# Performance work log

Hardware: AMD Instinct MI355X
Metric: run time of the kernel (lower is better)

## Reference

```python
import jax, jax.numpy as jnp
import numpy as np

NUM_EMBEDDINGS = 4096
EMBEDDING_DIM = 64
COMMITMENT_COST = 0.25
DECAY = 0.99
EPS = 1e-5


def setup_inputs() -> dict:
    key = jax.random.key(0)
    k1, k2, k3 = jax.random.split(key, 3)
    z = jax.random.normal(k1, (32, 1024, EMBEDDING_DIM), dtype=jnp.float32)
    # codebook initialized uniform(-1/K, 1/K) in the original; use small-scale normal-equivalent uniform
    embedding = jax.random.uniform(k2, (NUM_EMBEDDINGS, EMBEDDING_DIM), dtype=jnp.float32,
                                   minval=-1.0 / NUM_EMBEDDINGS, maxval=1.0 / NUM_EMBEDDINGS)
    ema_cluster_size = jnp.zeros((NUM_EMBEDDINGS,), dtype=jnp.float32)
    ema_w = embedding  # buffer initialized as a clone of the weight
    return {"z": z, "embedding": embedding, "ema_cluster_size": ema_cluster_size, "ema_w": ema_w}


def reference(z, embedding, ema_cluster_size, ema_w):
    B, T, D = z.shape
    K = embedding.shape[0]
    z_flat = z.reshape(-1, D)  # [N, D], N = B*T

    # squared L2 distances: ||z||^2 + ||e||^2 - 2 z e^T  -> [N, K]
    d = (jnp.sum(z_flat * z_flat, axis=1, keepdims=True)
         + jnp.sum(embedding * embedding, axis=1)
         - 2.0 * jnp.einsum('nd,kd->nk', z_flat, embedding))
    indices = jnp.argmin(d, axis=1)  # [N]

    z_q = embedding[indices].reshape(B, T, D)

    # EMA codebook update (training path); segment_sum == one-hot matmul, without
    # materializing the [N, K] one-hot matrix.
    counts = jax.ops.segment_sum(jnp.ones_like(indices, dtype=jnp.float32), indices,
                                 num_segments=K)  # encodings.sum(0)
    dw = jax.ops.segment_sum(z_flat, indices, num_segments=K)  # (z_flat^T @ encodings)^T -> [K, D]
    new_cluster_size = DECAY * ema_cluster_size + (1.0 - DECAY) * counts
    new_ema_w = DECAY * ema_w + (1.0 - DECAY) * dw
    n = jnp.sum(new_cluster_size)
    cluster_size = (new_cluster_size + EPS) / (n + K * EPS) * n
    new_embedding = new_ema_w / cluster_size[:, None]

    commitment_loss = COMMITMENT_COST * jnp.mean((z - jax.lax.stop_gradient(z_q)) ** 2)
    z_q_st = z + jax.lax.stop_gradient(z_q - z)  # straight-through estimator
    return (z_q_st, indices.reshape(B, T), commitment_loss,
            new_embedding, new_cluster_size, new_ema_w)
```

## Files before the change

kernel.cpp:

```cpp
#include <hip/hip_runtime.h>

#define N_ROWS 32768
#define K_EMB  4096
#define D_DIM  64
#define MARGIN 5e-4f
#define CAND_CAP 16
#define NQ      4
#define KC_CH   256
#define CH_PER  (K_EMB / NQ / KC_CH)

#define WS_EE     0
#define WS_BEST   4096
#define WS_IDX    69632
#define WS_COUNTS 102400
#define WS_DW     106496
#define WS_LOSS   368640
#define WS_N      368641
#define F_BHI     368644
#define F_BLO     499716
#define F_ROWMIN  630788
#define F_CNT     663556
#define F_CAND    696324
#define WS_NEED_BYTES ((size_t)(696324 + 32768 * CAND_CAP) * 4)

#define O_ZQ    0
#define O_IDX   2097152
#define O_LOSS  2129920
#define O_EMB   2129921
#define O_CS    2392065
#define O_EMAW  2396161

typedef __attribute__((ext_vector_type(8))) short short8;
typedef __attribute__((ext_vector_type(4))) float f32x4;

__device__ __forceinline__ unsigned short f2bf(float f) {
    unsigned u = __float_as_uint(f);
    unsigned r = (u + 0x7FFFu + ((u >> 16) & 1u)) >> 16;
    return (unsigned short)r;
}
__device__ __forceinline__ unsigned keyf(float f) {
    unsigned u = __float_as_uint(f);
    return (u & 0x80000000u) ? ~u : (u | 0x80000000u);
}
__device__ __forceinline__ float keyinv(unsigned k) {
    unsigned u = (k & 0x80000000u) ? (k ^ 0x80000000u) : ~k;
    return __uint_as_float(u);
}

__global__ void k_ee(const float* __restrict__ emb, float* __restrict__ ee) {
    int k = blockIdx.x * 256 + threadIdx.x;
    const float4* e4 = (const float4*)(emb + (size_t)k * D_DIM);
    float s0 = 0.f, s1 = 0.f, s2 = 0.f, s3 = 0.f;
#pragma unroll
    for (int i = 0; i < 16; ++i) {
        float4 v = e4[i];
        s0 = fmaf(v.x, v.x, s0);
        s1 = fmaf(v.y, v.y, s1);
        s2 = fmaf(v.z, v.z, s2);
        s3 = fmaf(v.w, v.w, s3);
    }
    ee[k] = (s0 + s1) + (s2 + s3);
}

__global__ void k_prep(const float* __restrict__ emb, float* __restrict__ ee,
                       unsigned short* __restrict__ bhi)
{
    int k = blockIdx.x * 256 + threadIdx.x;
    const float4* e4 = (const float4*)(emb + (size_t)k * D_DIM);
    float s0 = 0.f, s1 = 0.f, s2 = 0.f, s3 = 0.f;
    unsigned short* bh = bhi + (size_t)k * D_DIM;
#pragma unroll
    for (int i = 0; i < 16; ++i) {
        float4 v = e4[i];
        s0 = fmaf(v.x, v.x, s0);
        s1 = fmaf(v.y, v.y, s1);
        s2 = fmaf(v.z, v.z, s2);
        s3 = fmaf(v.w, v.w, s3);
        bh[4 * i + 0] = f2bf(v.x);
        bh[4 * i + 1] = f2bf(v.y);
        bh[4 * i + 2] = f2bf(v.z);
        bh[4 * i + 3] = f2bf(v.w);
    }
    ee[k] = (s0 + s1) + (s2 + s3);
}

template <int PASS>
__global__ __launch_bounds__(256, 2) void k_mfma_pass(
    const float* __restrict__ z, const unsigned short* __restrict__ bhi,
    const float* __restrict__ ee,
    unsigned* __restrict__ rowmin, unsigned* __restrict__ cnt, int* __restrict__ cand)
{
    __shared__ unsigned short lds_b[KC_CH * 64];
    __shared__ float lds_e2[KC_CH];

    const int tid  = threadIdx.x;
    const int lane = tid & 63, wave = tid >> 6;
    const int lrow = lane & 15, lgrp = lane >> 4;
    const int row0   = blockIdx.x * 256 + wave * 64;
    const int kquart = blockIdx.y * (K_EMB / NQ);

    short8 Ah[4][2];
#pragma unroll
    for (int s = 0; s < 4; ++s) {
#pragma unroll
        for (int t = 0; t < 2; ++t) {
            const float* zp = z + (size_t)(row0 + s * 16 + lrow) * D_DIM + t * 32 + lgrp * 8;
            float4 f0 = *(const float4*)zp;
            float4 f1 = *(const float4*)(zp + 4);
            float zf[8] = {f0.x, f0.y, f0.z, f0.w, f1.x, f1.y, f1.z, f1.w};
            short8 h;
#pragma unroll
            for (int j = 0; j < 8; ++j) h[j] = (short)f2bf(zf[j]);
            Ah[s][t] = h;
        }
    }

    float track[4][4];
#pragma unroll
    for (int s = 0; s < 4; ++s)
#pragma unroll
        for (int r = 0; r < 4; ++r) {
            track[s][r] = (PASS == 1)
                ? -3.4e38f
                : -0.5f * (keyinv(rowmin[row0 + s * 16 + lgrp * 4 + r]) + MARGIN);
        }

    const int swz = lrow & 7;

    for (int ch = 0; ch < CH_PER; ++ch) {
        const int kbase = kquart + ch * KC_CH;

        __syncthreads();
        {
            const short8* gsrc = (const short8*)(bhi + (size_t)kbase * D_DIM);
            short8 v[8];
#pragma unroll
            for (int j = 0; j < 8; ++j) v[j] = gsrc[tid + j * 256];
            const int s_slot = tid & 7, c0 = tid >> 3;
#pragma unroll
            for (int j = 0; j < 8; ++j) {
                int c = c0 + j * 32;
                *(short8*)&lds_b[c * 64 + ((s_slot ^ (c & 7)) << 3)] = v[j];
            }
            lds_e2[tid & (KC_CH - 1)] = -0.5f * ee[kbase + (tid & (KC_CH - 1))];
        }
        __syncthreads();

#pragma unroll 2
        for (int kt = 0; kt < KC_CH / 32; ++kt) {
            short8 B0[2], B1[2];
            float  e2[2];
#pragma unroll
            for (int u = 0; u < 2; ++u) {
                const int c = kt * 32 + u * 16 + lrow;
                B0[u] = *(const short8*)&lds_b[c * 64 + ((lgrp ^ swz) << 3)];
                B1[u] = *(const short8*)&lds_b[c * 64 + (((lgrp + 4) ^ swz) << 3)];
                e2[u] = lds_e2[c];
            }
#pragma unroll
            for (int s = 0; s < 4; ++s) {
#pragma unroll
                for (int u = 0; u < 2; ++u) {
                    f32x4 acc = {e2[u], e2[u], e2[u], e2[u]};
                    acc = __builtin_amdgcn_mfma_f32_16x16x32_bf16(Ah[s][0], B0[u], acc, 0, 0, 0);
                    acc = __builtin_amdgcn_mfma_f32_16x16x32_bf16(Ah[s][1], B1[u], acc, 0, 0, 0);
#pragma unroll
                    for (int r = 0; r < 4; ++r) {
                        if (PASS == 1) {
                            track[s][r] = fmaxf(track[s][r], acc[r]);
                        } else {
                            if (acc[r] > track[s][r]) {
                                int row = row0 + s * 16 + lgrp * 4 + r;
                                unsigned slot = atomicAdd(&cnt[row], 1u);
                                if (slot < (unsigned)CAND_CAP)
                                    cand[(size_t)row * CAND_CAP + slot] =
                                        kbase + kt * 32 + u * 16 + lrow;
                            }
                        }
                    }
                }
            }
        }
    }

    if (PASS == 1) {
#pragma unroll
        for (int s = 0; s < 4; ++s)
#pragma unroll
            for (int r = 0; r < 4; ++r) {
                float v = track[s][r];
                v = fmaxf(v, __shfl_xor(v, 1));
                v = fmaxf(v, __shfl_xor(v, 2));
                v = fmaxf(v, __shfl_xor(v, 4));
                v = fmaxf(v, __shfl_xor(v, 8));
                if (lrow == 0)
                    atomicMin(&rowmin[row0 + s * 16 + lgrp * 4 + r], keyf(-2.0f * v));
            }
    }
}

__global__ void k_refine(const float* __restrict__ z, const float* __restrict__ emb,
                         const float* __restrict__ ee, const unsigned* __restrict__ cnt,
                         const int* __restrict__ cand, unsigned long long* __restrict__ best)
{
    int row = blockIdx.x * 256 + threadIdx.x;
    const float4* zp = (const float4*)(z + (size_t)row * D_DIM);

    float s0 = 0.f, s1 = 0.f, s2 = 0.f, s3 = 0.f;
#pragma unroll
    for (int i = 0; i < 16; ++i) {
        float4 v = zp[i];
        s0 = fmaf(v.x, v.x, s0);
        s1 = fmaf(v.y, v.y, s1);
        s2 = fmaf(v.z, v.z, s2);
        s3 = fmaf(v.w, v.w, s3);
    }
    const float zz = (s0 + s1) + (s2 + s3);

    int c = (int)cnt[row];
    if (c > CAND_CAP) c = CAND_CAP;
    unsigned long long bk = 0xFFFFFFFFFFFFFFFFull;
    for (int i = 0; i < c; ++i) {
        int k = cand[(size_t)row * CAND_CAP + i];
        const float4* ep = (const float4*)(emb + (size_t)k * D_DIM);
        float d0 = 0.f, d1 = 0.f, d2 = 0.f, d3 = 0.f;
#pragma unroll
        for (int j = 0; j < 16; ++j) {
            float4 zv = zp[j];
            float4 ev = ep[j];
            d0 = fmaf(zv.x, ev.x, d0);
            d1 = fmaf(zv.y, ev.y, d1);
            d2 = fmaf(zv.z, ev.z, d2);
            d3 = fmaf(zv.w, ev.w, d3);
        }
        float dot = (d0 + d1) + (d2 + d3);
        float dv  = fmaf(-2.0f, dot, zz + ee[k]);
        unsigned long long key =
            ((unsigned long long)__float_as_uint(dv) << 32) | (unsigned)k;
        bk = (key < bk) ? key : bk;
    }
    best[row] = bk;
}

#define NCHUNK_FB 16
#define KC_FB     (K_EMB / NCHUNK_FB)
__global__ __launch_bounds__(256) void k_argmin_fb(
    const float* __restrict__ z, const float* __restrict__ emb,
    const float* __restrict__ ee, unsigned long long* __restrict__ best)
{
    const int n  = blockIdx.x * 256 + threadIdx.x;
    const int c  = blockIdx.y;
    const int k0 = c * KC_FB;

    float4 zr[16];
    const float4* zp = (const float4*)(z + (size_t)n * D_DIM);
#pragma unroll
    for (int i = 0; i < 16; ++i) zr[i] = zp[i];

    float s0 = 0.f, s1 = 0.f, s2 = 0.f, s3 = 0.f;
#pragma unroll
    for (int i = 0; i < 16; ++i) {
        s0 = fmaf(zr[i].x, zr[i].x, s0);
        s1 = fmaf(zr[i].y, zr[i].y, s1);
        s2 = fmaf(zr[i].z, zr[i].z, s2);
        s3 = fmaf(zr[i].w, zr[i].w, s3);
    }
    const float zz = (s0 + s1) + (s2 + s3);

    const float4* ep  = (const float4*)(emb + (size_t)k0 * D_DIM);
    const float*  eep = ee + k0;

    float bestv = 3.4e38f;
    int   bi    = 0;
#pragma unroll 2
    for (int kk = 0; kk < KC_FB; ++kk) {
        float d0 = 0.f, d1 = 0.f, d2 = 0.f, d3 = 0.f;
#pragma unroll
        for (int i = 0; i < 16; ++i) {
            float4 ev = ep[kk * 16 + i];
            d0 = fmaf(zr[i].x, ev.x, d0);
            d1 = fmaf(zr[i].y, ev.y, d1);
            d2 = fmaf(zr[i].z, ev.z, d2);
            d3 = fmaf(zr[i].w, ev.w, d3);
        }
        float dot = (d0 + d1) + (d2 + d3);
        float dv = fmaf(-2.0f, dot, zz + eep[kk]);
        if (dv < bestv) { bestv = dv; bi = kk; }
    }
    unsigned long long key =
        ((unsigned long long)__float_as_uint(bestv) << 32) | (unsigned)(k0 + bi);
    atomicMin(best + n, key);
}

__global__ void k_finish(const unsigned long long* __restrict__ best,
                         int* __restrict__ idxbuf, float* __restrict__ oidx)
{
    int n = blockIdx.x * 256 + threadIdx.x;
    int bi = (int)(best[n] & 0xFFFFFFFFull);
    idxbuf[n] = bi;
    oidx[n]   = (float)bi;
}

__global__ void k_scatter(const float* __restrict__ z, const float* __restrict__ emb,
                          const int* __restrict__ idxbuf, float* __restrict__ out_zq,
                          float* __restrict__ counts, float* __restrict__ dw,
                          float* __restrict__ lossacc)
{
    int t = blockIdx.x * 256 + threadIdx.x;
    float acc = 0.f;
#pragma unroll
    for (int i = 0; i < 16; ++i) {
        int e = t + i * 131072;
        int nrow = e >> 6, d = e & 63;
        int k = idxbuf[nrow];
        float zv  = z[e];
        float evv = emb[(size_t)k * D_DIM + d];
        out_zq[e] = zv + (evv - zv);
        float diff = zv - evv;
        acc = fmaf(diff, diff, acc);
        atomicAdd(&dw[(size_t)k * D_DIM + d], zv);
        if (d == 0) atomicAdd(&counts[k], 1.0f);
    }
    __shared__ float red[256];
    red[threadIdx.x] = acc;
    __syncthreads();
    for (int s = 128; s > 0; s >>= 1) {
        if (threadIdx.x < s) red[threadIdx.x] += red[threadIdx.x + s];
        __syncthreads();
    }
    if (threadIdx.x == 0) atomicAdd(lossacc, red[0]);
}

__global__ void k_stats(const float* __restrict__ ema_cs, const float* __restrict__ counts,
                        const float* __restrict__ lossacc, float* __restrict__ out_cs,
                        float* __restrict__ out_loss, float* __restrict__ ws_n)
{
    __shared__ float red[256];
    float local = 0.f;
    for (int k = threadIdx.x; k < K_EMB; k += 256) {
        float v = 0.99f * ema_cs[k] + 0.01f * counts[k];
        out_cs[k] = v;
        local += v;
    }
    red[threadIdx.x] = local;
    __syncthreads();
    for (int s = 128; s > 0; s >>= 1) {
        if (threadIdx.x < s) red[threadIdx.x] += red[threadIdx.x + s];
        __syncthreads();
    }
    if (threadIdx.x == 0) {
        ws_n[0] = red[0];
        out_loss[0] = 0.25f * (lossacc[0] / 2097152.0f);
    }
}

__global__ void k_emb(const float* __restrict__ ema_w, const float* __restrict__ dw,
                      const float* __restrict__ out_cs, const float* __restrict__ ws_n,
                      float* __restrict__ out_emb, float* __restrict__ out_emaw)
{
    int e = blockIdx.x * 256 + threadIdx.x;
    int k = e >> 6;
    float nv = ws_n[0];
    float w  = 0.99f * ema_w[e] + 0.01f * dw[e];
    out_emaw[e] = w;
    float cs = (out_cs[k] + 1e-5f) / (nv + 0.04096f) * nv;
    out_emb[e] = w / cs;
}

extern "C" void kernel_launch(void* const* d_in, const int* in_sizes, int n_in,
                              void* d_out, int out_size, void* d_ws, size_t ws_size,
                              hipStream_t stream)
{
    const float* z      = (const float*)d_in[0];
    const float* emb    = (const float*)d_in[1];
    const float* ema_cs = (const float*)d_in[2];
    const float* ema_w  = (const float*)d_in[3];

    float* out   = (float*)d_out;
    float* o_zq  = out + O_ZQ;
    float* o_idx = out + O_IDX;
    float* o_ls  = out + O_LOSS;
    float* o_em  = out + O_EMB;
    float* o_cs  = out + O_CS;
    float* o_ew  = out + O_EMAW;

    float* w      = (float*)d_ws;
    float* ee     = w + WS_EE;
    unsigned long long* best = (unsigned long long*)(w + WS_BEST);
    int*   idxbuf = (int*)(w + WS_IDX);
    float* counts = w + WS_COUNTS;
    float* dw     = w + WS_DW;
    float* lossa  = w + WS_LOSS;
    float* ws_n   = w + WS_N;

    hipMemsetAsync((char*)d_ws + (size_t)WS_BEST * 4, 0xFF, (size_t)N_ROWS * 8, stream);
    hipMemsetAsync((char*)d_ws + (size_t)WS_COUNTS * 4, 0,
                   (size_t)(WS_N + 1 - WS_COUNTS) * 4, stream);

    if (ws_size >= WS_NEED_BYTES) {
        unsigned short* bhi = (unsigned short*)(w + F_BHI);
        unsigned* rowmin    = (unsigned*)(w + F_ROWMIN);
        unsigned* cnt       = (unsigned*)(w + F_CNT);
        int*      cand      = (int*)(w + F_CAND);

        hipMemsetAsync((char*)d_ws + (size_t)F_ROWMIN * 4, 0xFF, (size_t)N_ROWS * 4, stream);
        hipMemsetAsync((char*)d_ws + (size_t)F_CNT * 4, 0, (size_t)N_ROWS * 4, stream);

        k_prep<<<K_EMB / 256, 256, 0, stream>>>(emb, ee, bhi);
        k_mfma_pass<1><<<dim3(N_ROWS / 256, NQ), 256, 0, stream>>>(z, bhi, ee,
                                                                   rowmin, cnt, cand);
        k_mfma_pass<2><<<dim3(N_ROWS / 256, NQ), 256, 0, stream>>>(z, bhi, ee,
                                                                   rowmin, cnt, cand);
        k_refine<<<N_ROWS / 256, 256, 0, stream>>>(z, emb, ee, cnt, cand, best);
    } else {
        k_ee<<<K_EMB / 256, 256, 0, stream>>>(emb, ee);
        k_argmin_fb<<<dim3(N_ROWS / 256, NCHUNK_FB), 256, 0, stream>>>(z, emb, ee, best);
    }

    k_finish<<<N_ROWS / 256, 256, 0, stream>>>(best, idxbuf, o_idx);
    k_scatter<<<512, 256, 0, stream>>>(z, emb, idxbuf, o_zq, counts, dw, lossa);
    k_stats<<<1, 256, 0, stream>>>(ema_cs, counts, lossa, o_cs, o_ls, ws_n);
    k_emb<<<(K_EMB * D_DIM) / 256, 256, 0, stream>>>(ema_w, dw, o_cs, ws_n, o_em, o_ew);
}
```

Baseline: 159.7 us.

## Fuse two MFMA distance passes into one kernel with per-quarter thresholds and rescue path

The separate max-pass and candidate-pass kernels are merged into one k_scan kernel. It computes each row's local best within its codebook quarter, then rescans the same quarter and keeps candidates within a margin of that local best. This drops the global rowmin buffer, its memset, the atomicMin and one launch, and shrinks blocks to 128 rows with launch_bounds 3 for occupancy. Because thresholds are now per-quarter, more candidates can be emitted per row. Rows that overflow the candidate cap go to a rescue list and get an exact full-codebook argmin in a new k_rescue kernel, which adds atomic traffic and an extra launch.

```diff
diff --git a/kernel.cpp b/kernel.cpp
--- a/kernel.cpp
+++ b/kernel.cpp
@@ -5,9 +5,11 @@
 #define D_DIM  64
 #define MARGIN 5e-4f
 #define CAND_CAP 16
+#define RESCUE_CAP 2048
 #define NQ      4
 #define KC_CH   256
 #define CH_PER  (K_EMB / NQ / KC_CH)
+#define ROWS_BLK 128
 
 #define WS_EE     0
 #define WS_BEST   4096
@@ -18,7 +20,7 @@
 #define WS_N      368641
 #define F_BHI     368644
 #define F_BLO     499716
-#define F_ROWMIN  630788
+#define F_RESCUE  630788
 #define F_CNT     663556
 #define F_CAND    696324
 #define WS_NEED_BYTES ((size_t)(696324 + 32768 * CAND_CAP) * 4)
@@ -37,14 +39,6 @@
     unsigned u = __float_as_uint(f);
     unsigned r = (u + 0x7FFFu + ((u >> 16) & 1u)) >> 16;
     return (unsigned short)r;
-}
-__device__ __forceinline__ unsigned keyf(float f) {
-    unsigned u = __float_as_uint(f);
-    return (u & 0x80000000u) ? ~u : (u | 0x80000000u);
-}
-__device__ __forceinline__ float keyinv(unsigned k) {
-    unsigned u = (k & 0x80000000u) ? (k ^ 0x80000000u) : ~k;
-    return __uint_as_float(u);
 }
 
 __global__ void k_ee(const float* __restrict__ emb, float* __restrict__ ee) {
@@ -84,11 +78,10 @@
     ee[k] = (s0 + s1) + (s2 + s3);
 }
 
-template <int PASS>
-__global__ __launch_bounds__(256, 2) void k_mfma_pass(
+__global__ __launch_bounds__(256, 3) void k_scan(
     const float* __restrict__ z, const unsigned short* __restrict__ bhi,
     const float* __restrict__ ee,
-    unsigned* __restrict__ rowmin, unsigned* __restrict__ cnt, int* __restrict__ cand)
+    unsigned* __restrict__ cnt, int* __restrict__ cand, unsigned* __restrict__ rescue)
 {
     __shared__ unsigned short lds_b[KC_CH * 64];
     __shared__ float lds_e2[KC_CH];
@@ -96,12 +89,12 @@
     const int tid  = threadIdx.x;
     const int lane = tid & 63, wave = tid >> 6;
     const int lrow = lane & 15, lgrp = lane >> 4;
-    const int row0   = blockIdx.x * 256 + wave * 64;
-    const int kquart = blockIdx.y * (K_EMB / NQ);
-
-    short8 Ah[4][2];
-#pragma unroll
-    for (int s = 0; s < 4; ++s) {
+    const int row0  = blockIdx.x * ROWS_BLK + wave * 32;
+    const int qbase = blockIdx.y * (K_EMB / NQ);
+
+    short8 Ah[2][2];
+#pragma unroll
+    for (int s = 0; s < 2; ++s) {
 #pragma unroll
         for (int t = 0; t < 2; ++t) {
             const float* zp = z + (size_t)(row0 + s * 16 + lrow) * D_DIM + t * 32 + lgrp * 8;
@@ -115,21 +108,15 @@
         }
     }
 
-    float track[4][4];
-#pragma unroll
-    for (int s = 0; s < 4; ++s)
-#pragma unroll
-        for (int r = 0; r < 4; ++r) {
-            track[s][r] = (PASS == 1)
-                ? -3.4e38f
-                : -0.5f * (keyinv(rowmin[row0 + s * 16 + lgrp * 4 + r]) + MARGIN);
-        }
-
     const int swz = lrow & 7;
+    float track[2][4];
+#pragma unroll
+    for (int s = 0; s < 2; ++s)
+#pragma unroll
+        for (int r = 0; r < 4; ++r) track[s][r] = -3.4e38f;
 
     for (int ch = 0; ch < CH_PER; ++ch) {
-        const int kbase = kquart + ch * KC_CH;
-
+        const int kbase = qbase + ch * KC_CH;
         __syncthreads();
         {
             const short8* gsrc = (const short8*)(bhi + (size_t)kbase * D_DIM);
@@ -158,44 +145,84 @@
                 e2[u] = lds_e2[c];
             }
 #pragma unroll
-            for (int s = 0; s < 4; ++s) {
+            for (int s = 0; s < 2; ++s)
 #pragma unroll
                 for (int u = 0; u < 2; ++u) {
                     f32x4 acc = {e2[u], e2[u], e2[u], e2[u]};
                     acc = __builtin_amdgcn_mfma_f32_16x16x32_bf16(Ah[s][0], B0[u], acc, 0, 0, 0);
                     acc = __builtin_amdgcn_mfma_f32_16x16x32_bf16(Ah[s][1], B1[u], acc, 0, 0, 0);
 #pragma unroll
+                    for (int r = 0; r < 4; ++r)
+                        track[s][r] = fmaxf(track[s][r], acc[r]);
+                }
+        }
+    }
+
+    float limit[2][4];
+#pragma unroll
+    for (int s = 0; s < 2; ++s)
+#pragma unroll
+        for (int r = 0; r < 4; ++r) {
+            float v = track[s][r];
+            v = fmaxf(v, __shfl_xor(v, 1));
+            v = fmaxf(v, __shfl_xor(v, 2));
+            v = fmaxf(v, __shfl_xor(v, 4));
+            v = fmaxf(v, __shfl_xor(v, 8));
+            limit[s][r] = v - 0.5f * MARGIN;
+        }
+
+    for (int ch = 0; ch < CH_PER; ++ch) {
+        const int kbase = qbase + ch * KC_CH;
+        __syncthreads();
+        {
+            const short8* gsrc = (const short8*)(bhi + (size_t)kbase * D_DIM);
+            short8 v[8];
+#pragma unroll
+            for (int j = 0; j < 8; ++j) v[j] = gsrc[tid + j * 256];
+            const int s_slot = tid & 7, c0 = tid >> 3;
+#pragma unroll
+            for (int j = 0; j < 8; ++j) {
+                int c = c0 + j * 32;
+                *(short8*)&lds_b[c * 64 + ((s_slot ^ (c & 7)) << 3)] = v[j];
+            }
+            lds_e2[tid & (KC_CH - 1)] = -0.5f * ee[kbase + (tid & (KC_CH - 1))];
+        }
+        __syncthreads();
+
+#pragma unroll 2
+        for (int kt = 0; kt < KC_CH / 32; ++kt) {
+            short8 B0[2], B1[2];
+            float  e2[2];
+#pragma unroll
+            for (int u = 0; u < 2; ++u) {
+                const int c = kt * 32 + u * 16 + lrow;
+                B0[u] = *(const short8*)&lds_b[c * 64 + ((lgrp ^ swz) << 3)];
+                B1[u] = *(const short8*)&lds_b[c * 64 + (((lgrp + 4) ^ swz) << 3)];
+                e2[u] = lds_e2[c];
+            }
+#pragma unroll
+            for (int s = 0; s < 2; ++s)
+#pragma unroll
+                for (int u = 0; u < 2; ++u) {
+                    f32x4 acc = {e2[u], e2[u], e2[u], e2[u]};
+                    acc = __builtin_amdgcn_mfma_f32_16x16x32_bf16(Ah[s][0], B0[u], acc, 0, 0, 0);
+                    acc = __builtin_amdgcn_mfma_f32_16x16x32_bf16(Ah[s][1], B1[u], acc, 0, 0, 0);
+#pragma unroll
                     for (int r = 0; r < 4; ++r) {
-                        if (PASS == 1) {
-                            track[s][r] = fmaxf(track[s][r], acc[r]);
-                        } else {
-                            if (acc[r] > track[s][r]) {
-                                int row = row0 + s * 16 + lgrp * 4 + r;
-                                unsigned slot = atomicAdd(&cnt[row], 1u);
-                                if (slot < (unsigned)CAND_CAP)
-                                    cand[(size_t)row * CAND_CAP + slot] =
-                                        kbase + kt * 32 + u * 16 + lrow;
+                        if (acc[r] > limit[s][r]) {
+                            int row = row0 + s * 16 + lgrp * 4 + r;
+                            unsigned slot = atomicAdd(&cnt[row], 1u);
+                            if (slot < (unsigned)CAND_CAP) {
+                                cand[(size_t)row * CAND_CAP + slot] =
+                                    kbase + kt * 32 + u * 16 + lrow;
+                            } else if (slot == (unsigned)CAND_CAP) {
+                                unsigned li = atomicAdd(rescue, 1u);
+                                if (li < (unsigned)RESCUE_CAP) rescue[1 + li] = (unsigned)row;
                             }
                         }
                     }
                 }
-            }
-        }
-    }
-
-    if (PASS == 1) {
-#pragma unroll
-        for (int s = 0; s < 4; ++s)
-#pragma unroll
-            for (int r = 0; r < 4; ++r) {
-                float v = track[s][r];
-                v = fmaxf(v, __shfl_xor(v, 1));
-                v = fmaxf(v, __shfl_xor(v, 2));
-                v = fmaxf(v, __shfl_xor(v, 4));
-                v = fmaxf(v, __shfl_xor(v, 8));
-                if (lrow == 0)
-                    atomicMin(&rowmin[row0 + s * 16 + lgrp * 4 + r], keyf(-2.0f * v));
-            }
+        }
     }
 }
 
@@ -240,6 +267,57 @@
         bk = (key < bk) ? key : bk;
     }
     best[row] = bk;
+}
+
+__global__ void k_rescue(const float* __restrict__ z, const float* __restrict__ emb,
+                         const float* __restrict__ ee, const unsigned* __restrict__ rescue,
+                         unsigned long long* __restrict__ best)
+{
+    int gw   = (blockIdx.x * 256 + threadIdx.x) >> 6;
+    int lane = threadIdx.x & 63;
+    unsigned nr = rescue[0];
+    if (nr > (unsigned)RESCUE_CAP) nr = RESCUE_CAP;
+    if (gw >= (int)nr) return;
+    int row = (int)rescue[1 + gw];
+
+    const float4* zp = (const float4*)(z + (size_t)row * D_DIM);
+    float s0 = 0.f, s1 = 0.f, s2 = 0.f, s3 = 0.f;
+#pragma unroll
+    for (int i = 0; i < 16; ++i) {
+        float4 v = zp[i];
+        s0 = fmaf(v.x, v.x, s0);
+        s1 = fmaf(v.y, v.y, s1);
+        s2 = fmaf(v.z, v.z, s2);
+        s3 = fmaf(v.w, v.w, s3);
+    }
+    const float zz = (s0 + s1) + (s2 + s3);
+
+    unsigned long long bk = 0xFFFFFFFFFFFFFFFFull;
+    for (int i = 0; i < K_EMB / 64; ++i) {
+        int k = i * 64 + lane;
+        const float4* ep = (const float4*)(emb + (size_t)k * D_DIM);
+        float d0 = 0.f, d1 = 0.f, d2 = 0.f, d3 = 0.f;
+#pragma unroll
+        for (int j = 0; j < 16; ++j) {
+            float4 zv = zp[j];
+            float4 ev = ep[j];
+            d0 = fmaf(zv.x, ev.x, d0);
+            d1 = fmaf(zv.y, ev.y, d1);
+            d2 = fmaf(zv.z, ev.z, d2);
+            d3 = fmaf(zv.w, ev.w, d3);
+        }
+        float dot = (d0 + d1) + (d2 + d3);
+        float dv  = fmaf(-2.0f, dot, zz + ee[k]);
+        unsigned long long key =
+            ((unsigned long long)__float_as_uint(dv) << 32) | (unsigned)k;
+        bk = (key < bk) ? key : bk;
+    }
+#pragma unroll
+    for (int m = 1; m <= 32; m <<= 1) {
+        unsigned long long o = __shfl_xor(bk, m);
+        bk = (o < bk) ? o : bk;
+    }
+    if (lane == 0) best[row] = bk;
 }
 
 #define NCHUNK_FB 16
@@ -399,19 +477,18 @@
 
     if (ws_size >= WS_NEED_BYTES) {
         unsigned short* bhi = (unsigned short*)(w + F_BHI);
-        unsigned* rowmin    = (unsigned*)(w + F_ROWMIN);
+        unsigned* rescue    = (unsigned*)(w + F_RESCUE);
         unsigned* cnt       = (unsigned*)(w + F_CNT);
         int*      cand      = (int*)(w + F_CAND);
 
-        hipMemsetAsync((char*)d_ws + (size_t)F_ROWMIN * 4, 0xFF, (size_t)N_ROWS * 4, stream);
-        hipMemsetAsync((char*)d_ws + (size_t)F_CNT * 4, 0, (size_t)N_ROWS * 4, stream);
+        hipMemsetAsync((char*)d_ws + (size_t)F_RESCUE * 4, 0,
+                       (size_t)(F_CAND - F_RESCUE) * 4, stream);
 
         k_prep<<<K_EMB / 256, 256, 0, stream>>>(emb, ee, bhi);
-        k_mfma_pass<1><<<dim3(N_ROWS / 256, NQ), 256, 0, stream>>>(z, bhi, ee,
-                                                                   rowmin, cnt, cand);
-        k_mfma_pass<2><<<dim3(N_ROWS / 256, NQ), 256, 0, stream>>>(z, bhi, ee,
-                                                                   rowmin, cnt, cand);
+        k_scan<<<dim3(N_ROWS / ROWS_BLK, NQ), 256, 0, stream>>>(z, bhi, ee, cnt, cand,
+                                                                rescue);
         k_refine<<<N_ROWS / 256, 256, 0, stream>>>(z, emb, ee, cnt, cand, best);
+        k_rescue<<<RESCUE_CAP / 4, 256, 0, stream>>>(z, emb, ee, rescue, best);
     } else {
         k_ee<<<K_EMB / 256, 256, 0, stream>>>(emb, ee);
         k_argmin_fb<<<dim3(N_ROWS / 256, NCHUNK_FB), 256, 0, stream>>>(z, emb, ee, best);
```

Measured after the change: 277.3 us. 73.6% more time.
